# Kernel optimization log

Measured on AMD Instinct MI355X. Metric: run time of the kernel, lower is better.

Reference implementation:

```python
import jax, jax.numpy as jnp
import numpy as np

B, S, D, H = 64, 512, 1024, 1024

def setup_inputs() -> dict:
    key = jax.random.key(0)
    ks = jax.random.split(key, 7)
    s = 1.0 / np.sqrt(H)
    return {
        "x": jax.random.normal(ks[0], (B, S, D), dtype=jnp.float32),
        "h0": jax.random.normal(ks[1], (H,), dtype=jnp.float32),
        "c0": jax.random.normal(ks[2], (H,), dtype=jnp.float32),
        "Wi": jax.random.normal(ks[3], (4 * H, D), dtype=jnp.float32) * s,
        "bi": jax.random.normal(ks[4], (4 * H,), dtype=jnp.float32) * s,
        "Wh": jax.random.normal(ks[5], (4 * H, H), dtype=jnp.float32) * s,
        "bh": jax.random.normal(ks[6], (4 * H,), dtype=jnp.float32) * s,
    }

def reference(x, h0, c0, Wi, bi, Wh, bh):
    # x: [B,S,D]; h0,c0: [H] broadcast over batch (matches torch zeros(H) semantics)
    b, _, _ = x.shape
    h = jnp.broadcast_to(h0, (b, H))
    c = jnp.broadcast_to(c0, (b, H))
    # Precompute the input projection for all timesteps in one big GEMM (same math).
    xg = jnp.einsum('bsd,gd->bsg', x, Wi) + bi  # [B,S,4H]

    def step(carry, xg_t):
        h, c = carry
        gates = xg_t + h @ Wh.T + bh  # [B,4H]
        i = jax.nn.sigmoid(gates[:, :H])
        f = jax.nn.sigmoid(gates[:, H:2 * H])
        g = jnp.tanh(gates[:, 2 * H:3 * H])
        o = jax.nn.sigmoid(gates[:, 3 * H:])
        c = f * c + i * g
        h = o * jnp.tanh(c)
        return (h, c), h

    (h, c), hs = jax.lax.scan(step, (h, c), jnp.swapaxes(xg, 0, 1))  # hs: [S,B,H]
    hidden_seq = jnp.swapaxes(hs, 0, 1)  # [B,S,H]
    return hidden_seq, (h, c)
```

## Files before the change

kernel.cpp:

```cpp
#include <hip/hip_runtime.h>
#include <cstdint>
#include <cstddef>

#define B_ 64
#define S_ 512
#define D_ 1024
#define H_ 1024
#define G_ 4096
#define NBLK 256

typedef short short8 __attribute__((ext_vector_type(8)));
typedef float floatx4 __attribute__((ext_vector_type(4)));

__device__ __forceinline__ unsigned short bf16_rne(float f) {
  union { float f; unsigned u; } v; v.f = f;
  return (unsigned short)((v.u + 0x7FFFu + ((v.u >> 16) & 1u)) >> 16);
}
__device__ __forceinline__ float sigf(float x) { return 1.0f / (1.0f + __expf(-x)); }
__device__ __forceinline__ float tanhf_fast(float x) {
  float e = __expf(2.0f * x);
  return 1.0f - 2.0f / (e + 1.0f);
}

__device__ __forceinline__ void astore64(void* p, uint64_t v) {
  __hip_atomic_store((unsigned long long*)p, (unsigned long long)v,
                     __ATOMIC_RELAXED, __HIP_MEMORY_SCOPE_AGENT);
}
__device__ __forceinline__ void cpoll64(uint4* a, uint4* b, uint4* c, uint4* d, const void* p) {
  asm volatile("global_load_dwordx4 %0, %4, off sc0 sc1\n\t"
               "global_load_dwordx4 %1, %4, off offset:16 sc0 sc1\n\t"
               "global_load_dwordx4 %2, %4, off offset:32 sc0 sc1\n\t"
               "global_load_dwordx4 %3, %4, off offset:48 sc0 sc1\n\t"
               "s_waitcnt vmcnt(0)"
               : "=&v"(*a), "=&v"(*b), "=&v"(*c), "=&v"(*d)
               : "v"(p) : "memory");
}

#define BARRIER_LGKM() do {                                   \
    asm volatile("s_waitcnt lgkmcnt(0)" ::: "memory");        \
    __builtin_amdgcn_s_barrier();                             \
    asm volatile("" ::: "memory");                            \
  } while (0)

__global__ void f32_to_bf16_k(const float* __restrict__ s, unsigned short* __restrict__ d, int n) {
  int i = (blockIdx.x * 256 + threadIdx.x) * 4;
  if (i < n) {
    float4 v = *(const float4*)(s + i);
    ushort4 o;
    o.x = bf16_rne(v.x); o.y = bf16_rne(v.y); o.z = bf16_rne(v.z); o.w = bf16_rne(v.w);
    *(ushort4*)(d + i) = o;
  }
}

__global__ void bsum_k(const float* __restrict__ bi, const float* __restrict__ bh, float* __restrict__ o) {
  int i = blockIdx.x * 256 + threadIdx.x;
  if (i < G_) o[i] = bi[i] + bh[i];
}

__global__ void hinit_k(const float* __restrict__ h0, unsigned* __restrict__ hb32) {
  int i = blockIdx.x * 256 + threadIdx.x;
  if (i < B_ * H_) hb32[i] = ((unsigned)bf16_rne(h0[i & (H_ - 1)])) << 16;
}

__global__ __launch_bounds__(256, 3) void gemm_xg(
    const unsigned short* __restrict__ xa,
    const unsigned short* __restrict__ wb,
    const float* __restrict__ bsum,
    void* __restrict__ xgv, int xg16)
{
  __shared__ unsigned short As[128 * 72];
  __shared__ unsigned short Bs[128 * 72];
  const int tid = threadIdx.x, ln = tid & 63, wv = tid >> 6;
  const int q = ln >> 4, lr = ln & 15;
  const int bid = blockIdx.x;
  const int nt = bid & 31, mt = bid >> 5;
  const int m0 = mt << 7, n0 = nt << 7;
  const int wm = (wv & 1) << 6, wn = (wv >> 1) << 6;
  floatx4 acc[4][4] = {};

  for (int kk = 0; kk < 1024; kk += 64) {
    __syncthreads();
#pragma unroll
    for (int i = 0; i < 4; i++) {
      int f = i * 256 + tid;
      int row = f >> 3, c8 = (f & 7) << 3;
      short8 va = *(const short8*)(xa + (size_t)(m0 + row) * 1024 + kk + c8);
      short8 vb = *(const short8*)(wb + (size_t)(n0 + row) * 1024 + kk + c8);
      *(short8*)(As + row * 72 + c8) = va;
      *(short8*)(Bs + row * 72 + c8) = vb;
    }
    __syncthreads();
#pragma unroll
    for (int ks = 0; ks < 2; ks++) {
      short8 af[4], bf[4];
#pragma unroll
      for (int mi = 0; mi < 4; mi++)
        af[mi] = *(const short8*)(As + (wm + mi * 16 + lr) * 72 + ks * 32 + q * 8);
#pragma unroll
      for (int ni = 0; ni < 4; ni++)
        bf[ni] = *(const short8*)(Bs + (wn + ni * 16 + lr) * 72 + ks * 32 + q * 8);
#pragma unroll
      for (int mi = 0; mi < 4; mi++)
#pragma unroll
        for (int ni = 0; ni < 4; ni++)
          acc[mi][ni] = __builtin_amdgcn_mfma_f32_16x16x32_bf16(af[mi], bf[ni], acc[mi][ni], 0, 0, 0);
    }
  }
  const int b = m0 >> 9, s0 = m0 & 511;
#pragma unroll
  for (int mi = 0; mi < 4; mi++) {
#pragma unroll
    for (int r = 0; r < 4; r++) {
      int mrow = wm + mi * 16 + q * 4 + r;
      size_t base = (size_t)(s0 + mrow) * (B_ * G_) + (size_t)b * G_;
#pragma unroll
      for (int ni = 0; ni < 4; ni++) {
        int n = n0 + wn + ni * 16 + lr;
        float v = acc[mi][ni][r] + bsum[n];
        if (xg16) ((unsigned short*)xgv)[base + n] = bf16_rne(v);
        else      ((float*)xgv)[base + n] = v;
      }
    }
  }
}

__global__ __launch_bounds__(1024, 1) void lstm_rec(
    const void* __restrict__ xgv, int xg16,
    const unsigned short* __restrict__ wh,
    unsigned* __restrict__ hb32,
    const float* __restrict__ c0,
    float* __restrict__ out_hid,
    float* __restrict__ out_h,
    float* __restrict__ out_c)
{
  __shared__ unsigned short hs[16 * 1032];
  __shared__ float red[3][4][16][16];
  __shared__ unsigned short hout_bf[256];
  __shared__ float hout_f[256];

  const int tid = threadIdx.x, ln = tid & 63, wv = tid >> 6;
  const int nt = wv & 3, kt = wv >> 2;
  const int bid = blockIdx.x, bg = bid & 3, cg = bid >> 2;
  const int r0 = bg << 4, j0 = cg << 4;
  const int nloc = ln & 15, q = ln >> 4;
  const int tg = nloc >> 2, u = nloc & 3;
  const int j = j0 + (nt << 2) + u;
  const int gcol = tg * 1024 + j;

  short8 bfr[8];
#pragma unroll
  for (int s8 = 0; s8 < 8; s8++)
    bfr[s8] = *(const short8*)(wh + (size_t)gcol * 1024 + kt * 256 + s8 * 32 + q * 8);

  float cst[4];
#pragma unroll
  for (int r = 0; r < 4; r++) cst[r] = c0[j];

  const int srow = tid >> 6, scc = (tid & 63) << 4;

  for (int t = 0; t < 512; t++) {
    float xv[4] = {0.f, 0.f, 0.f, 0.f};
    if (kt == 0) {
      const size_t xbase = (size_t)t * (B_ * G_) + (size_t)r0 * G_ + gcol;
      if (xg16) {
#pragma unroll
        for (int r = 0; r < 4; r++) {
          unsigned short w = ((const unsigned short*)xgv)[xbase + (size_t)(q * 4 + r) * G_];
          union { unsigned uu; float ff; } cv; cv.uu = ((unsigned)w) << 16; xv[r] = cv.ff;
        }
      } else {
#pragma unroll
        for (int r = 0; r < 4; r++)
          xv[r] = ((const float*)xgv)[xbase + (size_t)(q * 4 + r) * G_];
      }
    }

    {
      const unsigned* hp = hb32 + (size_t)(t & 1) * (B_ * H_)
                         + ((size_t)(r0 + srow) << 10) + scc;
      const unsigned tg16 = (unsigned)t & 0xffffu;
      uint4 w0, w1, w2, w3;
      for (;;) {
        cpoll64(&w0, &w1, &w2, &w3, hp);
        unsigned dv = ((w0.x ^ tg16) | (w0.y ^ tg16) | (w0.z ^ tg16) | (w0.w ^ tg16)
                     | (w1.x ^ tg16) | (w1.y ^ tg16) | (w1.z ^ tg16) | (w1.w ^ tg16)
                     | (w2.x ^ tg16) | (w2.y ^ tg16) | (w2.z ^ tg16) | (w2.w ^ tg16)
                     | (w3.x ^ tg16) | (w3.y ^ tg16) | (w3.z ^ tg16) | (w3.w ^ tg16)) & 0xffffu;
        if (dv == 0) break;
        __builtin_amdgcn_s_sleep(2);
      }
      unsigned* hd = (unsigned*)(hs + srow * 1032 + scc);
      hd[0] = (w0.x >> 16) | (w0.y & 0xffff0000u);
      hd[1] = (w0.z >> 16) | (w0.w & 0xffff0000u);
      hd[2] = (w1.x >> 16) | (w1.y & 0xffff0000u);
      hd[3] = (w1.z >> 16) | (w1.w & 0xffff0000u);
      hd[4] = (w2.x >> 16) | (w2.y & 0xffff0000u);
      hd[5] = (w2.z >> 16) | (w2.w & 0xffff0000u);
      hd[6] = (w3.x >> 16) | (w3.y & 0xffff0000u);
      hd[7] = (w3.z >> 16) | (w3.w & 0xffff0000u);
    }
    __syncthreads();

    floatx4 acc = {0.f, 0.f, 0.f, 0.f};
#pragma unroll
    for (int s8 = 0; s8 < 8; s8++) {
      short8 af = *(const short8*)(hs + nloc * 1032 + kt * 256 + s8 * 32 + q * 8);
      acc = __builtin_amdgcn_mfma_f32_16x16x32_bf16(af, bfr[s8], acc, 0, 0, 0);
    }
    if (kt) {
#pragma unroll
      for (int r = 0; r < 4; r++) red[kt - 1][nt][q * 4 + r][nloc] = acc[r];
    }
    __syncthreads();

    if (kt == 0) {
      float gv[4];
#pragma unroll
      for (int r = 0; r < 4; r++)
        gv[r] = acc[r] + red[0][nt][q * 4 + r][nloc] + red[1][nt][q * 4 + r][nloc]
              + red[2][nt][q * 4 + r][nloc] + xv[r];
      const int sb = q << 4;
#pragma unroll
      for (int r = 0; r < 4; r++) {
        float vi = __shfl(gv[r], sb + u);
        float vf = __shfl(gv[r], sb + 4 + u);
        float vg = __shfl(gv[r], sb + 8 + u);
        float vo = __shfl(gv[r], sb + 12 + u);
        float i_ = sigf(vi), f_ = sigf(vf), g_ = tanhf_fast(vg), o_ = sigf(vo);
        float cn = f_ * cst[r] + i_ * g_;
        cst[r] = cn;
        float hn = o_ * tanhf_fast(cn);
        if (tg == 0) {
          int m = (q << 2) + r;
          hout_bf[(m << 4) + (nt << 2) + u] = bf16_rne(hn);
          hout_f [(m << 4) + (nt << 2) + u] = hn;
          if (t == 511) {
            int brow = r0 + m;
            out_h[(brow << 10) + j] = hn;
            out_c[(brow << 10) + j] = cn;
          }
        }
      }
    }
    __syncthreads();

    if (wv == 0) {
      if (t < 511) {
        unsigned* hw32 = hb32 + (size_t)((t + 1) & 1) * (B_ * H_);
        const int row = ln >> 2, c4 = (ln & 3) << 2;
        const uint64_t tag = (unsigned)(t + 1);
        const unsigned short* hb4 = hout_bf + (row << 4) + c4;
        uint64_t w01 = ((((uint64_t)hb4[0] << 16) | tag))
                     | ((((uint64_t)hb4[1] << 16) | tag) << 32);
        uint64_t w23 = ((((uint64_t)hb4[2] << 16) | tag))
                     | ((((uint64_t)hb4[3] << 16) | tag) << 32);
        unsigned* dst = hw32 + ((size_t)(r0 + row) << 10) + j0 + c4;
        astore64(dst, w01);
        astore64(dst + 2, w23);
      }
    } else if (wv == 1) {
      int row = ln >> 2, c4 = (ln & 3) << 2;
      float4 fv = *(const float4*)(hout_f + (row << 4) + c4);
      *(float4*)(out_hid + (size_t)(r0 + row) * (S_ * H_) + (size_t)t * H_ + j0 + c4) = fv;
    }
    BARRIER_LGKM();
  }
}

extern "C" void kernel_launch(void* const* d_in, const int* in_sizes, int n_in,
                              void* d_out, int out_size, void* d_ws, size_t ws_size,
                              hipStream_t stream) {
  const float* x  = (const float*)d_in[0];
  const float* h0 = (const float*)d_in[1];
  const float* c0 = (const float*)d_in[2];
  const float* Wi = (const float*)d_in[3];
  const float* bi = (const float*)d_in[4];
  const float* Wh = (const float*)d_in[5];
  const float* bh = (const float*)d_in[6];

  float* out_hid = (float*)d_out;
  float* out_h = out_hid + (size_t)B_ * S_ * H_;
  float* out_c = out_h + (size_t)B_ * H_;

  uint8_t* ws = (uint8_t*)d_ws;
  const size_t xg_fp32 = (size_t)S_ * B_ * G_ * 4;
  const size_t xg_bf16 = (size_t)S_ * B_ * G_ * 2;
  const size_t xbf_b = (size_t)B_ * S_ * D_ * 2;
  const size_t w_b = (size_t)G_ * D_ * 2;
  const size_t hb_b = (size_t)2 * B_ * H_ * 4;
  const size_t rest = xbf_b + 2 * w_b + (size_t)G_ * 4 + hb_b + 8192;
  int xg16 = (ws_size >= xg_fp32 + rest) ? 0 : 1;
  size_t xg_bytes = xg16 ? xg_bf16 : xg_fp32;

  size_t off = 0;
  void* xg = (void*)(ws + off);                      off += xg_bytes;
  unsigned short* xbf = (unsigned short*)(ws + off); off += xbf_b;
  unsigned short* wib = (unsigned short*)(ws + off); off += w_b;
  unsigned short* whb = (unsigned short*)(ws + off); off += w_b;
  float* bsum = (float*)(ws + off);                  off += (size_t)G_ * 4;
  unsigned* hb32 = (unsigned*)(ws + off);            off += hb_b;

  hipMemsetAsync(hb32, 0xFF, hb_b, stream);
  f32_to_bf16_k<<<(B_ * S_ * D_ / 4 + 255) / 256, 256, 0, stream>>>(x, xbf, B_ * S_ * D_);
  f32_to_bf16_k<<<(G_ * D_ / 4 + 255) / 256, 256, 0, stream>>>(Wi, wib, G_ * D_);
  f32_to_bf16_k<<<(G_ * D_ / 4 + 255) / 256, 256, 0, stream>>>(Wh, whb, G_ * D_);
  bsum_k<<<G_ / 256, 256, 0, stream>>>(bi, bh, bsum);
  hinit_k<<<(B_ * H_ + 255) / 256, 256, 0, stream>>>(h0, hb32);

  gemm_xg<<<dim3((S_ * B_ / 128) * (G_ / 128)), 256, 0, stream>>>(xbf, wib, bsum, xg, xg16);

  void* args[] = { (void*)&xg, (void*)&xg16, (void*)&whb, (void*)&hb32, (void*)&c0,
                   (void*)&out_hid, (void*)&out_h, (void*)&out_c };
  hipLaunchCooperativeKernel((void*)lstm_rec, dim3(NBLK), dim3(1024), args, 0, stream);
}
```

Before: 3.445 ms.

## Replace end-of-step barrier with per-batch-group arrival counters and direct stores

Drops the LDS staging of h outputs and the trailing block barrier. Each gate lane now writes its tagged bf16 h value and its fp32 hidden output straight to global memory. A per-batch-group arrival array is added: wave 0 of each block polls the 64 counters of its group before reading h, and the block publishes its own counter after the step. The aim is to shorten the per-step critical path by removing a barrier and the staging copies. The cost is an extra polling phase per step, scattered 4-byte stores instead of vectorised ones, and memory-ordering risk because the counter store is relaxed and not fenced after the h stores from other lanes.

New measurement: 3.414 ms. Within noise of the previous version (-0.9%).

```diff
diff --git a/kernel.cpp b/kernel.cpp
--- a/kernel.cpp
+++ b/kernel.cpp
@@ -22,9 +22,11 @@
   return 1.0f - 2.0f / (e + 1.0f);
 }
 
-__device__ __forceinline__ void astore64(void* p, uint64_t v) {
-  __hip_atomic_store((unsigned long long*)p, (unsigned long long)v,
-                     __ATOMIC_RELAXED, __HIP_MEMORY_SCOPE_AGENT);
+__device__ __forceinline__ void astore32(unsigned* p, unsigned v) {
+  __hip_atomic_store(p, v, __ATOMIC_RELAXED, __HIP_MEMORY_SCOPE_AGENT);
+}
+__device__ __forceinline__ unsigned aload32(const unsigned* p) {
+  return __hip_atomic_load(p, __ATOMIC_RELAXED, __HIP_MEMORY_SCOPE_AGENT);
 }
 __device__ __forceinline__ void cpoll64(uint4* a, uint4* b, uint4* c, uint4* d, const void* p) {
   asm volatile("global_load_dwordx4 %0, %4, off sc0 sc1\n\t"
@@ -131,12 +133,11 @@
     const float* __restrict__ c0,
     float* __restrict__ out_hid,
     float* __restrict__ out_h,
-    float* __restrict__ out_c)
+    float* __restrict__ out_c,
+    unsigned* __restrict__ arr)
 {
   __shared__ unsigned short hs[16 * 1032];
   __shared__ float red[3][4][16][16];
-  __shared__ unsigned short hout_bf[256];
-  __shared__ float hout_f[256];
 
   const int tid = threadIdx.x, ln = tid & 63, wv = tid >> 6;
   const int nt = wv & 3, kt = wv >> 2;
@@ -147,6 +148,8 @@
   const int j = j0 + (nt << 2) + u;
   const int gcol = tg * 1024 + j;
 
+  unsigned* arr_bg = arr + (bg << 6);
+
   short8 bfr[8];
 #pragma unroll
   for (int s8 = 0; s8 < 8; s8++)
@@ -174,6 +177,16 @@
           xv[r] = ((const float*)xgv)[xbase + (size_t)(q * 4 + r) * G_];
       }
     }
+
+    if (wv == 0) {
+      const unsigned tgt = (unsigned)t;
+      for (;;) {
+        unsigned v = aload32(arr_bg + ln);
+        if (__all((int)(v >= tgt))) break;
+        __builtin_amdgcn_s_sleep(1);
+      }
+    }
+    BARRIER_LGKM();
 
     {
       const unsigned* hp = hb32 + (size_t)(t & 1) * (B_ * H_)
@@ -219,6 +232,7 @@
       for (int r = 0; r < 4; r++)
         gv[r] = acc[r] + red[0][nt][q * 4 + r][nloc] + red[1][nt][q * 4 + r][nloc]
               + red[2][nt][q * 4 + r][nloc] + xv[r];
+      unsigned* hw32 = hb32 + (size_t)((t + 1) & 1) * (B_ * H_);
       const int sb = q << 4;
 #pragma unroll
       for (int r = 0; r < 4; r++) {
@@ -231,39 +245,19 @@
         cst[r] = cn;
         float hn = o_ * tanhf_fast(cn);
         if (tg == 0) {
-          int m = (q << 2) + r;
-          hout_bf[(m << 4) + (nt << 2) + u] = bf16_rne(hn);
-          hout_f [(m << 4) + (nt << 2) + u] = hn;
-          if (t == 511) {
-            int brow = r0 + m;
-            out_h[(brow << 10) + j] = hn;
-            out_c[(brow << 10) + j] = cn;
+          const int m = (q << 2) + r;
+          out_hid[(size_t)(r0 + m) * (S_ * H_) + (size_t)t * H_ + j] = hn;
+          if (t < 511) {
+            unsigned pv = (((unsigned)bf16_rne(hn)) << 16) | (unsigned)(t + 1);
+            astore32(hw32 + (((size_t)(r0 + m)) << 10) + j, pv);
+          } else {
+            out_h[((r0 + m) << 10) + j] = hn;
+            out_c[((r0 + m) << 10) + j] = cn;
           }
         }
       }
-    }
-    __syncthreads();
-
-    if (wv == 0) {
-      if (t < 511) {
-        unsigned* hw32 = hb32 + (size_t)((t + 1) & 1) * (B_ * H_);
-        const int row = ln >> 2, c4 = (ln & 3) << 2;
-        const uint64_t tag = (unsigned)(t + 1);
-        const unsigned short* hb4 = hout_bf + (row << 4) + c4;
-        uint64_t w01 = ((((uint64_t)hb4[0] << 16) | tag))
-                     | ((((uint64_t)hb4[1] << 16) | tag) << 32);
-        uint64_t w23 = ((((uint64_t)hb4[2] << 16) | tag))
-                     | ((((uint64_t)hb4[3] << 16) | tag) << 32);
-        unsigned* dst = hw32 + ((size_t)(r0 + row) << 10) + j0 + c4;
-        astore64(dst, w01);
-        astore64(dst + 2, w23);
-      }
-    } else if (wv == 1) {
-      int row = ln >> 2, c4 = (ln & 3) << 2;
-      float4 fv = *(const float4*)(hout_f + (row << 4) + c4);
-      *(float4*)(out_hid + (size_t)(r0 + row) * (S_ * H_) + (size_t)t * H_ + j0 + c4) = fv;
-    }
-    BARRIER_LGKM();
+      if (wv == 0 && ln == 0 && t < 511) astore32(arr_bg + cg, (unsigned)(t + 1));
+    }
   }
 }
 
@@ -299,7 +293,10 @@
   unsigned short* whb = (unsigned short*)(ws + off); off += w_b;
   float* bsum = (float*)(ws + off);                  off += (size_t)G_ * 4;
   unsigned* hb32 = (unsigned*)(ws + off);            off += hb_b;
-
+  off = (off + 255) & ~(size_t)255;
+  unsigned* arrp = (unsigned*)(ws + off);
+
+  hipMemsetAsync(arrp, 0, 4096, stream);
   hipMemsetAsync(hb32, 0xFF, hb_b, stream);
   f32_to_bf16_k<<<(B_ * S_ * D_ / 4 + 255) / 256, 256, 0, stream>>>(x, xbf, B_ * S_ * D_);
   f32_to_bf16_k<<<(G_ * D_ / 4 + 255) / 256, 256, 0, stream>>>(Wi, wib, G_ * D_);
@@ -310,6 +307,6 @@
   gemm_xg<<<dim3((S_ * B_ / 128) * (G_ / 128)), 256, 0, stream>>>(xbf, wib, bsum, xg, xg16);
 
   void* args[] = { (void*)&xg, (void*)&xg16, (void*)&whb, (void*)&hb32, (void*)&c0,
-                   (void*)&out_hid, (void*)&out_h, (void*)&out_c };
+                   (void*)&out_hid, (void*)&out_h, (void*)&out_c, (void*)&arrp };
   hipLaunchCooperativeKernel((void*)lstm_rec, dim3(NBLK), dim3(1024), args, 0, stream);
 }
```
